# Kernel tuning notes

Measured on AMD Instinct MI355X. Metric: run time of the kernel, lower is better.

The kernel has to match this reference:

```python
import jax, jax.numpy as jnp
import numpy as np
from jax import lax

CUT = 20            # voxel grid per side, hard-coded in the torch module
N, P, OP = 32, 8192, 2048


def _w(key, shape, fan_in):
    return jax.random.normal(key, shape, dtype=jnp.float32) * np.float32(1.0 / np.sqrt(fan_in))


def setup_inputs() -> dict:
    key = jax.random.key(0)
    ks = jax.random.split(key, 20)
    inp = {}
    inp["sc"] = jax.random.uniform(ks[0], (N, P, 2), dtype=jnp.float32, minval=-0.5, maxval=0.5)
    inp["oc"] = jax.random.uniform(ks[1], (N, OP, 2), dtype=jnp.float32, minval=-0.5, maxval=0.5)
    inp["pos"] = jax.random.uniform(ks[2], (N, 2), dtype=jnp.float32, minval=-0.5, maxval=0.5)
    # voxel PointNet MLP (1x1 Conv1d == per-point linear)
    inp["mlp_w1"] = _w(ks[3], (128, 2), 2);        inp["mlp_b1"] = jnp.zeros((128,), jnp.float32)
    inp["mlp_w2"] = _w(ks[4], (256, 128), 128);    inp["mlp_b2"] = jnp.zeros((256,), jnp.float32)
    # dense conv pyramid
    inp["conv1_w"] = _w(ks[5], (512, 256, 3, 3), 256 * 9);   inp["conv1_b"] = jnp.zeros((512,), jnp.float32)
    inp["conv2_w"] = _w(ks[6], (1024, 512, 3, 3), 512 * 9);  inp["conv2_b"] = jnp.zeros((1024,), jnp.float32)
    inp["convt_w"] = _w(ks[7], (512, 1024, 2, 2), 1024 * 4); inp["convt_b"] = jnp.zeros((512,), jnp.float32)
    # object set-abstraction (stack of 1x1 Conv1d)
    inp["sa_w1"] = _w(ks[8], (64, 2), 2);          inp["sa_b1"] = jnp.zeros((64,), jnp.float32)
    inp["sa_w2"] = _w(ks[9], (128, 64), 64);       inp["sa_b2"] = jnp.zeros((128,), jnp.float32)
    inp["sa_w3"] = _w(ks[10], (256, 128), 128);    inp["sa_b3"] = jnp.zeros((256,), jnp.float32)
    inp["sa_w4"] = _w(ks[11], (512, 256), 256);    inp["sa_b4"] = jnp.zeros((512,), jnp.float32)
    # per-cell classifier
    inp["cls_w1"] = _w(ks[12], (1024, 1538), 1538); inp["cls_b1"] = jnp.zeros((1024,), jnp.float32)
    inp["cls_w2"] = _w(ks[13], (256, 1024), 1024);  inp["cls_b2"] = jnp.zeros((256,), jnp.float32)
    inp["cls_w3"] = _w(ks[14], (1, 256), 256);      inp["cls_b3"] = jnp.zeros((1,), jnp.float32)
    return inp


def _conv2d(x, w, b):
    y = lax.conv_general_dilated(x, w, (1, 1), ((1, 1), (1, 1)),
                                 dimension_numbers=("NCHW", "OIHW", "NCHW"))
    return y + b[None, :, None, None]


def _maxpool2(x):
    return lax.reduce_window(x, -jnp.inf, lax.max, (1, 1, 2, 2), (1, 1, 2, 2), "VALID")


def reference(sc, oc, pos,
              mlp_w1, mlp_b1, mlp_w2, mlp_b2,
              conv1_w, conv1_b, conv2_w, conv2_b, convt_w, convt_b,
              sa_w1, sa_b1, sa_w2, sa_b2, sa_w3, sa_b3, sa_w4, sa_b4,
              cls_w1, cls_b1, cls_w2, cls_b2, cls_w3, cls_b3):
    n = sc.shape[0]
    # ---- fused voxelization + PointNet + scatter-max (replaces triple loop) ----
    x, y = sc[..., 0], sc[..., 1]
    # torch condition: cut[i] < x <= cut[i+1] on linspace(-0.5, 0.5, 21)
    bi = jnp.clip(jnp.ceil((x + 0.5) * CUT) - 1, 0, CUT - 1).astype(jnp.int32)
    bj = jnp.clip(jnp.ceil((y + 0.5) * CUT) - 1, 0, CUT - 1).astype(jnp.int32)
    valid = (x > -0.5) & (x <= 0.5) & (y > -0.5) & (y <= 0.5)
    ci = -0.5 + (bi.astype(sc.dtype) + 0.5) / CUT   # voxel center x
    cj = -0.5 + (bj.astype(sc.dtype) + 0.5) / CUT   # voxel center y
    pc = jnp.stack([x - ci, y - cj], axis=-1).reshape(-1, 2)        # [n*P, 2]
    h = jax.nn.relu(pc @ mlp_w1.T + mlp_b1)
    feat = jax.nn.relu(h @ mlp_w2.T + mlp_b2)                       # [n*P, 256]
    seg = jnp.where(valid,
                    jnp.arange(n, dtype=jnp.int32)[:, None] * (CUT * CUT) + bi * CUT + bj,
                    n * CUT * CUT).reshape(-1)                      # invalid -> dummy bin
    nseg = n * CUT * CUT + 1
    mx = jax.ops.segment_max(feat, seg, num_segments=nseg)
    cnt = jax.ops.segment_sum(jnp.ones((n * P,), jnp.float32), seg, num_segments=nseg)
    vox = jnp.where(cnt[:, None] > 0, mx, 0.0)[: n * CUT * CUT]     # empty voxels stay 0
    vox = vox.reshape(n, CUT, CUT, 256).transpose(0, 3, 1, 2)       # [n,256,20,20]
    # ---- dense conv pyramid ----
    f1 = _maxpool2(jax.nn.relu(_conv2d(vox, conv1_w, conv1_b)))     # [n,512,10,10]
    f2 = _maxpool2(jax.nn.relu(_conv2d(f1, conv2_w, conv2_b)))      # [n,1024,5,5]
    f3 = lax.conv_transpose(f2, convt_w, (2, 2), "VALID",
                            dimension_numbers=("NCHW", "OIHW", "NCHW"))
    f3 = f3 + convt_b[None, :, None, None]                          # [n,512,10,10]
    scene = jnp.concatenate([f1, f3], axis=1)                       # [n,1024,10,10]
    S = scene.shape[2]
    scene_flat = scene.reshape(n, 1024, S * S)
    # ---- object PointNet (1x1 convs == per-point linears) + global max ----
    obj_c = oc - jnp.mean(oc, axis=1, keepdims=True)                # [n,OP,2]
    g = jax.nn.relu(obj_c @ sa_w1.T + sa_b1)
    g = jax.nn.relu(g @ sa_w2.T + sa_b2)
    g = jax.nn.relu(g @ sa_w3.T + sa_b3)
    g = jax.nn.relu(g @ sa_w4.T + sa_b4)                            # [n,OP,512]
    obj = jnp.max(g, axis=1)                                        # [n,512]
    obj_tiled = jnp.broadcast_to(obj[:, :, None], (n, 512, S * S))
    # ---- relative position grid ----
    c = -0.5 + (jnp.arange(S, dtype=sc.dtype) + 0.5) / S
    rel_x = jnp.broadcast_to(pos[:, 0][:, None, None] - c[None, :, None], (n, S, S))
    rel_y = jnp.broadcast_to(pos[:, 1][:, None, None] - c[None, None, :], (n, S, S))
    rel = jnp.stack([rel_x, rel_y], axis=1).reshape(n, 2, S * S)
    # ---- per-cell classifier ----
    cin = jnp.concatenate([scene_flat, obj_tiled, rel], axis=1).transpose(0, 2, 1)  # [n,100,1538]
    h = jax.nn.relu(cin @ cls_w1.T + cls_b1)
    h = jax.nn.relu(h @ cls_w2.T + cls_b2)
    return h @ cls_w3.T + cls_b3                                    # [n,100,1]
```

## Files before the change

kernel.cpp:

```cpp
#include <hip/hip_runtime.h>

#define NB 32
#define PP 8192
#define OPP 2048

typedef _Float16 f16;
typedef f16 half8 __attribute__((ext_vector_type(8)));
typedef f16 half4 __attribute__((ext_vector_type(4)));
typedef f16 half2v __attribute__((ext_vector_type(2)));
typedef float f32x4 __attribute__((ext_vector_type(4)));

#define MFMA16(a, b, c) __builtin_amdgcn_mfma_f32_16x16x32_f16(a, b, c, 0, 0, 0)

template <int CO, int CI>
__global__ __launch_bounds__(256) void wfragprep_k(const float* __restrict__ wsrc,
                                                   f16* __restrict__ wf) {
  __shared__ float tile[CI * 9];
  int co = blockIdx.x, t = threadIdx.x;
  const float* src = wsrc + (size_t)co * CI * 9;
  for (int i = t; i < CI * 9; i += 256) tile[i] = src[i];
  __syncthreads();
  constexpr int NBB = CO / 16;
  int nb = co >> 4, l16 = co & 15;
  for (int e = t; e < (CI / 32) * 9 * 4; e += 256) {
    int quad = e & 3;
    int kk = (e >> 2) % 9;
    int cic = e / 36;
    half8 v;
#pragma unroll
    for (int j = 0; j < 8; ++j) {
      int ci = cic * 32 + quad * 8 + j;
      v[j] = (f16)tile[ci * 9 + kk];
    }
    *(half8*)(wf + ((((size_t)cic * 9 + kk) * NBB + nb) * 64 + quad * 16 + l16) * 8) = v;
  }
}

__global__ void cvt16_k(const float* __restrict__ in, f16* __restrict__ out, int n4) {
  int idx = blockIdx.x * 256 + threadIdx.x;
  if (idx >= n4) return;
  float4 v = ((const float4*)in)[idx];
  half4 h; h.x = (f16)v.x; h.y = (f16)v.y; h.z = (f16)v.z; h.w = (f16)v.w;
  ((half4*)out)[idx] = h;
}

__global__ void cw1prep_k(const float* __restrict__ w, f16* __restrict__ out) {
  int idx = blockIdx.x * 256 + threadIdx.x;
  if (idx >= 1024 * 1024) return;
  int co = idx >> 10, k = idx & 1023;
  out[idx] = (f16)w[(size_t)co * 1538 + k];
}

__global__ void ctprep_k(const float* __restrict__ w, f16* __restrict__ out) {
  int idx = blockIdx.x * 256 + threadIdx.x;
  if (idx >= 2048 * 1024) return;
  int j = idx & 7, l = (idx >> 3) & 63, kb = (idx >> 9) & 31, nb = idx >> 14;
  int n16 = l & 15, quad = l >> 4;
  int np = nb * 16 + n16;
  int k = kb * 32 + quad * 8 + j;
  int p = np >> 9, o = np & 511;
  out[idx] = (f16)w[((size_t)o * 1024 + k) * 4 + (3 - p)];
}

__global__ void ocmean_k(const float* __restrict__ oc, float* __restrict__ ocm) {
  int n = blockIdx.x, t = threadIdx.x;
  __shared__ float sx[256], sy[256];
  float ax = 0.f, ay = 0.f;
  for (int p = t; p < OPP; p += 256) {
    ax += oc[((size_t)n * OPP + p) * 2 + 0];
    ay += oc[((size_t)n * OPP + p) * 2 + 1];
  }
  sx[t] = ax; sy[t] = ay;
  __syncthreads();
  for (int s = 128; s > 0; s >>= 1) {
    if (t < s) { sx[t] += sx[t + s]; sy[t] += sy[t + s]; }
    __syncthreads();
  }
  if (t == 0) {
    ocm[n * 2 + 0] = sx[0] / (float)OPP;
    ocm[n * 2 + 1] = sy[0] / (float)OPP;
  }
}

__global__ __launch_bounds__(256) void pointnet_lds_k(
    const float* __restrict__ sc, const float* __restrict__ w1, const float* __restrict__ b1,
    const f16* __restrict__ w2h, const float* __restrict__ b2, float* __restrict__ voxg) {
  __shared__ float voxl[400 * 33];
  int t = threadIdx.x, lane = t & 63, w = t >> 6;
  int quad = lane >> 4, l16 = lane & 15;
  int b = blockIdx.x;
  int ps = b & 3, cg = (b >> 2) & 7, n = b >> 5;
  half2v w1x2[16], w1y2[16], b12[16];
#pragma unroll
  for (int i = 0; i < 16; ++i) {
    int k0 = (i >> 2) * 32 + quad * 8 + (i & 3) * 2;
    w1x2[i] = (half2v){(f16)w1[k0 * 2], (f16)w1[(k0 + 1) * 2]};
    w1y2[i] = (half2v){(f16)w1[k0 * 2 + 1], (f16)w1[(k0 + 1) * 2 + 1]};
    b12[i]  = (half2v){(f16)b1[k0], (f16)b1[k0 + 1]};
  }
  half8 bf[2][4];
  float bias[2];
#pragma unroll
  for (int nt = 0; nt < 2; ++nt) {
    int ch = cg * 32 + nt * 16 + l16;
    bias[nt] = b2[ch];
#pragma unroll
    for (int ks = 0; ks < 4; ++ks)
      bf[nt][ks] = *(const half8*)(w2h + (size_t)ch * 128 + ks * 32 + quad * 8);
  }
  for (int i = t; i < 400 * 33; i += 256) voxl[i] = 0.0f;
  __syncthreads();
  const half2v z2 = {};
  const float* scp = sc + ((size_t)n * PP + (size_t)ps * 2048) * 2;
  int p0 = w * 16 + l16;
  float2 xy = *(const float2*)(scp + p0 * 2);
  for (int it = 0; it < 32; ++it) {
    float x = xy.x, y = xy.y;
    if (it < 31) xy = *(const float2*)(scp + ((it + 1) * 64 + p0) * 2);
    float bif = fminf(fmaxf(ceilf((x + 0.5f) * 20.0f) - 1.0f, 0.0f), 19.0f);
    float bjf = fminf(fmaxf(ceilf((y + 0.5f) * 20.0f) - 1.0f, 0.0f), 19.0f);
    bool valid = (x > -0.5f) && (x <= 0.5f) && (y > -0.5f) && (y <= 0.5f);
    float px = x - (-0.5f + (bif + 0.5f) * 0.05f);
    float py = y - (-0.5f + (bjf + 0.5f) * 0.05f);
    int bn = valid ? ((int)bif * 20 + (int)bjf) : -1;
    f16 pxh = (f16)px, pyh = (f16)py;
    half2v px2 = (half2v){pxh, pxh}, py2 = (half2v){pyh, pyh};
    f32x4 acc0 = {}, acc1 = {};
#pragma unroll
    for (int ks = 0; ks < 4; ++ks) {
      half8 af;
#pragma unroll
      for (int j2 = 0; j2 < 4; ++j2) {
        half2v tmp = w1x2[ks * 4 + j2] * px2 + (w1y2[ks * 4 + j2] * py2 + b12[ks * 4 + j2]);
        tmp = __builtin_elementwise_max(tmp, z2);
        reinterpret_cast<half2v*>(&af)[j2] = tmp;
      }
      acc0 = MFMA16(af, bf[0][ks], acc0);
      acc1 = MFMA16(af, bf[1][ks], acc1);
    }
#pragma unroll
    for (int r = 0; r < 4; ++r) {
      int bn2 = __shfl(bn, quad * 4 + r);
      if (bn2 >= 0) {
        float v0 = fmaxf(acc0[r] + bias[0], 0.0f);
        float v1 = fmaxf(acc1[r] + bias[1], 0.0f);
        atomicMax((int*)voxl + bn2 * 33 + l16, __float_as_int(v0));
        atomicMax((int*)voxl + bn2 * 33 + 16 + l16, __float_as_int(v1));
      }
    }
  }
  __syncthreads();
  float* vg = voxg + ((size_t)n * 400) * 256 + cg * 32;
  for (int i = t; i < 400 * 32; i += 256) {
    int bin = i >> 5, c = i & 31;
    float v = voxl[bin * 33 + c];
    if (v > 0.0f)
      atomicMax((int*)(vg + (size_t)bin * 256) + c, __float_as_int(v));
  }
}

template <int H, int W, int CI, int CO, int MSPLIT>
__global__ __launch_bounds__(256, 2) void convmfma_k(
    const f16* __restrict__ inh, const f16* __restrict__ wf,
    const float* __restrict__ bias, f16* __restrict__ outh) {
  constexpr int HS = H / MSPLIT;
  constexpr int Mpix = HS * W;
  constexpr int MT = (Mpix + 15) / 16;
  constexpr int PR = HS + 2, PC = W + 2;
  constexpr int NCIC = CI / 32;
  constexpr int COG = CO / 128;
  constexpr int NBB = CO / 16;
  extern __shared__ char smem[];
  f16* Ap = (f16*)smem;
  int b = blockIdx.x;
  int cog = b % COG;
  int ms = (b / COG) % MSPLIT;
  int n = b / (COG * MSPLIT);
  int co0 = cog * 128;
  int r0 = ms * HS;
  int t = threadIdx.x, lane = t & 63, w = t >> 6;
  int quad = lane >> 4, l16 = lane & 15;
  int nb0 = cog * 8 + w * 2;

  int abase[MT];
#pragma unroll
  for (int mi = 0; mi < MT; ++mi) {
    int pl = mi * 16 + l16; if (pl > Mpix - 1) pl = Mpix - 1;
    int y = pl / W, x = pl - y * W;
    abase[mi] = (y * PC + x) * 40 + quad * 8;
  }
  f32x4 acc[MT][2] = {};

  const f16* inbase = inh + (size_t)n * H * W * CI;

  for (int cic = 0; cic < NCIC; ++cic) {
    __syncthreads();
    for (int cell = t; cell < PR * PC; cell += 256) {
      int pr = cell / PC, pc = cell - pr * PC;
      int yin = r0 - 1 + pr, xin = pc - 1;
      uint4 d0 = {0,0,0,0}, d1 = {0,0,0,0}, d2 = {0,0,0,0}, d3 = {0,0,0,0};
      if (yin >= 0 && yin < H && xin >= 0 && xin < W) {
        const uint4* src = (const uint4*)(inbase + ((size_t)yin * W + xin) * CI + cic * 32);
        d0 = src[0]; d1 = src[1]; d2 = src[2]; d3 = src[3];
      }
      uint4* dst = (uint4*)(Ap + cell * 40);
      dst[0] = d0; dst[1] = d1; dst[2] = d2; dst[3] = d3;
    }
    __syncthreads();
    const f16* wfc = wf + (size_t)(cic * 9) * NBB * 512;
#pragma unroll
    for (int ky = 0; ky < 3; ++ky)
#pragma unroll
      for (int kx = 0; kx < 3; ++kx) {
        int kk = ky * 3 + kx;
        half8 bf0 = *(const half8*)(wfc + ((size_t)(kk * NBB + nb0) * 64 + lane) * 8);
        half8 bf1 = *(const half8*)(wfc + ((size_t)(kk * NBB + nb0 + 1) * 64 + lane) * 8);
        int shift = (ky * PC + kx) * 40;
#pragma unroll
        for (int mi = 0; mi < MT; ++mi) {
          half8 af = *(const half8*)(Ap + abase[mi] + shift);
          acc[mi][0] = MFMA16(af, bf0, acc[mi][0]);
          acc[mi][1] = MFMA16(af, bf1, acc[mi][1]);
        }
      }
  }
  int co_w = co0 + w * 32;
  float bv0 = bias[co_w + l16];
  float bv1 = bias[co_w + 16 + l16];
  f16* ob = outh + ((size_t)n * H * W + (size_t)ms * Mpix) * CO;
#pragma unroll
  for (int mi = 0; mi < MT; ++mi) {
#pragma unroll
    for (int r = 0; r < 4; ++r) {
      int p = mi * 16 + quad * 4 + r;
      if (p < Mpix) {
        float v0 = acc[mi][0][r] + bv0; v0 = v0 > 0.f ? v0 : 0.f;
        float v1 = acc[mi][1][r] + bv1; v1 = v1 > 0.f ? v1 : 0.f;
        ob[(size_t)p * CO + co_w + l16] = (f16)v0;
        ob[(size_t)p * CO + co_w + 16 + l16] = (f16)v1;
      }
    }
  }
}

__global__ void pool1_k(const f16* __restrict__ g1, f16* __restrict__ f1h,
                        f16* __restrict__ scnh) {
  int idx = blockIdx.x * 256 + threadIdx.x;
  if (idx >= 32 * 100 * 256) return;
  int c2 = idx & 255, rem = idx >> 8;
  int op = rem % 100, n = rem / 100;
  int py = op / 10, px = op - py * 10;
  const f16* base = g1 + (((size_t)n * 400 + (size_t)(2 * py) * 20 + 2 * px) * 512) + c2 * 2;
  float a0 = (float)base[0],   a1 = (float)base[1];
  float b0 = (float)base[512], b1 = (float)base[513];
  const f16* base2 = base + 20 * 512;
  float c0 = (float)base2[0],   c1 = (float)base2[1];
  float d0 = (float)base2[512], d1 = (float)base2[513];
  union { f16 h[2]; unsigned u; } pk;
  pk.h[0] = (f16)fmaxf(fmaxf(a0, b0), fmaxf(c0, d0));
  pk.h[1] = (f16)fmaxf(fmaxf(a1, b1), fmaxf(c1, d1));
  *(unsigned*)(f1h + ((size_t)n * 100 + op) * 512 + c2 * 2) = pk.u;
  *(unsigned*)(scnh + ((size_t)n * 100 + op) * 1024 + c2 * 2) = pk.u;
}

__global__ void pool2_k(const f16* __restrict__ g2, f16* __restrict__ f2h) {
  int idx = blockIdx.x * 256 + threadIdx.x;
  if (idx >= 32 * 25 * 512) return;
  int c2 = idx & 511, rem = idx >> 9;
  int op = rem % 25, n = rem / 25;
  int py = op / 5, px = op - py * 5;
  const f16* base = g2 + (((size_t)n * 100 + (size_t)(2 * py) * 10 + 2 * px) * 1024) + c2 * 2;
  float a0 = (float)base[0],    a1 = (float)base[1];
  float b0 = (float)base[1024], b1 = (float)base[1025];
  const f16* base2 = base + 10 * 1024;
  float c0 = (float)base2[0],    c1 = (float)base2[1];
  float d0 = (float)base2[1024], d1 = (float)base2[1025];
  f16* o = f2h + ((size_t)n * 25 + op) * 1024 + c2 * 2;
  o[0] = (f16)fmaxf(fmaxf(a0, b0), fmaxf(c0, d0));
  o[1] = (f16)fmaxf(fmaxf(a1, b1), fmaxf(c1, d1));
}

__global__ __launch_bounds__(256, 2) void convt_mfma_k(
    const f16* __restrict__ f2h, const f16* __restrict__ ctwf,
    const float* __restrict__ ctb, f16* __restrict__ scnh) {
  __shared__ f16 act[25 * 1048];
  int b = blockIdx.x;
  int ng = b & 15, n = b >> 4;
  int t = threadIdx.x, lane = t & 63, w = t >> 6;
  int quad = lane >> 4, l16 = lane & 15;
  for (int i = t; i < 25 * 128; i += 256) {
    int row = i >> 7, c8 = i & 127;
    *(half8*)(act + row * 1048 + c8 * 8) =
        *(const half8*)(f2h + ((size_t)n * 25 + row) * 1024 + c8 * 8);
  }
  __syncthreads();
  int r1 = 16 + (l16 > 8 ? 8 : l16);
  f32x4 acc[2][2] = {};
  const f16* wp0 = ctwf + ((size_t)((ng * 8 + w * 2 + 0) * 32) * 64 + lane) * 8;
  const f16* wp1 = ctwf + ((size_t)((ng * 8 + w * 2 + 1) * 32) * 64 + lane) * 8;
#pragma unroll 4
  for (int ks = 0; ks < 32; ++ks) {
    half8 a0 = *(const half8*)(act + l16 * 1048 + ks * 32 + quad * 8);
    half8 a1 = *(const half8*)(act + r1 * 1048 + ks * 32 + quad * 8);
    half8 b0 = *(const half8*)(wp0 + (size_t)ks * 512);
    half8 b1 = *(const half8*)(wp1 + (size_t)ks * 512);
    acc[0][0] = MFMA16(a0, b0, acc[0][0]);
    acc[1][0] = MFMA16(a1, b0, acc[1][0]);
    acc[0][1] = MFMA16(a0, b1, acc[0][1]);
    acc[1][1] = MFMA16(a1, b1, acc[1][1]);
  }
#pragma unroll
  for (int nt = 0; nt < 2; ++nt) {
    int np = ng * 128 + w * 32 + nt * 16 + l16;
    int p = np >> 9, co = np & 511;
    int a = p >> 1, bc = p & 1;
    float bb = ctb[co];
#pragma unroll
    for (int mt = 0; mt < 2; ++mt)
#pragma unroll
      for (int r = 0; r < 4; ++r) {
        int px = mt * 16 + quad * 4 + r;
        if (px < 25) {
          int ph = px / 5, pw = px - ph * 5;
          int opx = (2 * ph + a) * 10 + 2 * pw + bc;
          scnh[((size_t)n * 100 + opx) * 1024 + 512 + co] = (f16)(acc[mt][nt][r] + bb);
        }
      }
  }
}

__global__ __launch_bounds__(256, 2) void sa_mfma_k(
    const float* __restrict__ oc, const float* __restrict__ ocm,
    const float* __restrict__ w1, const float* __restrict__ b1,
    const f16* __restrict__ w2h, const float* __restrict__ b2,
    const f16* __restrict__ w3h, const float* __restrict__ b3,
    const f16* __restrict__ w4h, const float* __restrict__ b4,
    float* __restrict__ obj) {
  __shared__ f16 act1[64 * 72];
  __shared__ f16 act2[64 * 136];
  __shared__ f16 act3[64 * 264];
  __shared__ float pcx[64], pcy[64];
  int b = blockIdx.x;
  int n = b >> 5, pb = (b & 31) * 64;
  int t = threadIdx.x, lane = t & 63, w = t >> 6;
  int quad = lane >> 4, l16 = lane & 15;
  if (t < 64) {
    pcx[t] = oc[((size_t)n * OPP + pb + t) * 2 + 0] - ocm[n * 2 + 0];
    pcy[t] = oc[((size_t)n * OPP + pb + t) * 2 + 1] - ocm[n * 2 + 1];
  }
  __syncthreads();
  {
    int c = t & 63, pg = t >> 6;
    float wx = w1[c * 2], wy = w1[c * 2 + 1], bb = b1[c];
#pragma unroll
    for (int j = 0; j < 16; ++j) {
      int p = pg * 16 + j;
      act1[p * 72 + c] = (f16)fmaxf(fmaf(wx, pcx[p], fmaf(wy, pcy[p], bb)), 0.0f);
    }
  }
  __syncthreads();
  {
    int n0 = w * 32;
    f32x4 acc[4][2] = {};
#pragma unroll
    for (int ks = 0; ks < 2; ++ks) {
      half8 a[4];
#pragma unroll
      for (int mt = 0; mt < 4; ++mt)
        a[mt] = *(const half8*)(act1 + (mt * 16 + l16) * 72 + ks * 32 + quad * 8);
#pragma unroll
      for (int nt = 0; nt < 2; ++nt) {
        half8 bf = *(const half8*)(w2h + (size_t)(n0 + nt * 16 + l16) * 64 + ks * 32 + quad * 8);
#pragma unroll
        for (int mt = 0; mt < 4; ++mt)
          acc[mt][nt] = MFMA16(a[mt], bf, acc[mt][nt]);
      }
    }
#pragma unroll
    for (int nt = 0; nt < 2; ++nt) {
      int col = n0 + nt * 16 + l16;
      float bb = b2[col];
#pragma unroll
      for (int mt = 0; mt < 4; ++mt)
#pragma unroll
        for (int r = 0; r < 4; ++r)
          act2[(mt * 16 + quad * 4 + r) * 136 + col] = (f16)fmaxf(acc[mt][nt][r] + bb, 0.0f);
    }
  }
  __syncthreads();
  {
    int n0 = w * 64;
    f32x4 acc[4][4] = {};
#pragma unroll
    for (int ks = 0; ks < 4; ++ks) {
      half8 a[4];
#pragma unroll
      for (int mt = 0; mt < 4; ++mt)
        a[mt] = *(const half8*)(act2 + (mt * 16 + l16) * 136 + ks * 32 + quad * 8);
#pragma unroll
      for (int nt = 0; nt < 4; ++nt) {
        half8 bf = *(const half8*)(w3h + (size_t)(n0 + nt * 16 + l16) * 128 + ks * 32 + quad * 8);
#pragma unroll
        for (int mt = 0; mt < 4; ++mt)
          acc[mt][nt] = MFMA16(a[mt], bf, acc[mt][nt]);
      }
    }
#pragma unroll
    for (int nt = 0; nt < 4; ++nt) {
      int col = n0 + nt * 16 + l16;
      float bb = b3[col];
#pragma unroll
      for (int mt = 0; mt < 4; ++mt)
#pragma unroll
        for (int r = 0; r < 4; ++r)
          act3[(mt * 16 + quad * 4 + r) * 264 + col] = (f16)fmaxf(acc[mt][nt][r] + bb, 0.0f);
    }
  }
  __syncthreads();
  {
    int n0 = w * 128;
    f32x4 acc[4][8] = {};
#pragma unroll
    for (int ks = 0; ks < 8; ++ks) {
      half8 a[4];
#pragma unroll
      for (int mt = 0; mt < 4; ++mt)
        a[mt] = *(const half8*)(act3 + (mt * 16 + l16) * 264 + ks * 32 + quad * 8);
#pragma unroll
      for (int nt = 0; nt < 8; ++nt) {
        half8 bf = *(const half8*)(w4h + (size_t)(n0 + nt * 16 + l16) * 256 + ks * 32 + quad * 8);
#pragma unroll
        for (int mt = 0; mt < 4; ++mt)
          acc[mt][nt] = MFMA16(a[mt], bf, acc[mt][nt]);
      }
    }
#pragma unroll
    for (int nt = 0; nt < 8; ++nt) {
      int col = n0 + nt * 16 + l16;
      float bb = b4[col];
      float v = 0.0f;
#pragma unroll
      for (int mt = 0; mt < 4; ++mt)
#pragma unroll
        for (int r = 0; r < 4; ++r)
          v = fmaxf(v, acc[mt][nt][r] + bb);
      v = fmaxf(v, 0.0f);
      v = fmaxf(v, __shfl_xor(v, 16));
      v = fmaxf(v, __shfl_xor(v, 32));
      if (quad == 0)
        atomicMax((int*)obj + (size_t)n * 512 + col, __float_as_int(v));
    }
  }
}

__global__ __launch_bounds__(256) void cls1_mfma_k(
    const f16* __restrict__ scnh, const float* __restrict__ obj,
    const float* __restrict__ pos, const float* __restrict__ w1raw,
    const f16* __restrict__ w1h, const float* __restrict__ b1,
    f16* __restrict__ h1h) {
  __shared__ f16 act[112 * 72];
  __shared__ float objl[512];
  __shared__ float odl[128], wAl[128], wBl[128];
  int b = blockIdx.x;
  int o8 = b & 7, n = b >> 3;
  int co0 = o8 * 128;
  int t = threadIdx.x, lane = t & 63, w = t >> 6;
  int quad = lane >> 4, l16 = lane & 15;
  objl[t] = obj[(size_t)n * 512 + t];
  objl[t + 256] = obj[(size_t)n * 512 + t + 256];
  __syncthreads();
  if (t < 128) {
    int co = co0 + t;
    const float* wr = w1raw + (size_t)co * 1538;
    float od = 0.0f;
    for (int k = 0; k < 512; ++k) od = fmaf(objl[k], wr[1024 + k], od);
    odl[t] = od + b1[co];
    wAl[t] = wr[1536]; wBl[t] = wr[1537];
  }
  __syncthreads();
  float posx = pos[n * 2 + 0], posy = pos[n * 2 + 1];
  f32x4 acc[7][2];
#pragma unroll
  for (int mt = 0; mt < 7; ++mt)
#pragma unroll
    for (int nt = 0; nt < 2; ++nt) {
      int cl = w * 32 + nt * 16 + l16;
      float od = odl[cl], wA = wAl[cl], wB = wBl[cl];
#pragma unroll
      for (int r = 0; r < 4; ++r) {
        int px = mt * 16 + quad * 4 + r;
        float relx = posx - (-0.5f + ((px / 10) + 0.5f) * 0.1f);
        float rely = posy - (-0.5f + ((px % 10) + 0.5f) * 0.1f);
        acc[mt][nt][r] = od + relx * wA + rely * wB;
      }
    }
  for (int kc = 0; kc < 16; ++kc) {
    int k0 = kc * 64;
    __syncthreads();
    for (int i = t; i < 896; i += 256) {
      int row = i >> 3, c8 = i & 7;
      half8 v = {};
      if (row < 100) v = *(const half8*)(scnh + ((size_t)n * 100 + row) * 1024 + k0 + c8 * 8);
      *(half8*)(act + row * 72 + c8 * 8) = v;
    }
    __syncthreads();
#pragma unroll
    for (int ks = 0; ks < 2; ++ks) {
      half8 bf0 = *(const half8*)(w1h + (size_t)(co0 + w * 32 + l16) * 1024 + k0 + ks * 32 + quad * 8);
      half8 bf1 = *(const half8*)(w1h + (size_t)(co0 + w * 32 + 16 + l16) * 1024 + k0 + ks * 32 + quad * 8);
#pragma unroll
      for (int mt = 0; mt < 7; ++mt) {
        half8 a = *(const half8*)(act + (mt * 16 + l16) * 72 + ks * 32 + quad * 8);
        acc[mt][0] = MFMA16(a, bf0, acc[mt][0]);
        acc[mt][1] = MFMA16(a, bf1, acc[mt][1]);
      }
    }
  }
#pragma unroll
  for (int mt = 0; mt < 7; ++mt)
#pragma unroll
    for (int nt = 0; nt < 2; ++nt) {
      int co = co0 + w * 32 + nt * 16 + l16;
#pragma unroll
      for (int r = 0; r < 4; ++r) {
        int px = mt * 16 + quad * 4 + r;
        if (px < 100)
          h1h[((size_t)n * 100 + px) * 1024 + co] = (f16)fmaxf(acc[mt][nt][r], 0.0f);
      }
    }
}

__global__ __launch_bounds__(256) void cls2_mfma_k(
    const f16* __restrict__ h1h, const f16* __restrict__ w2h16,
    const float* __restrict__ b2, f16* __restrict__ h2h) {
  __shared__ f16 act[64 * 72];
  int b = blockIdx.x;
  int ng = b & 1, mh = (b >> 1) & 1, n = b >> 2;
  int co0 = ng * 128, p0 = mh * 50;
  int t = threadIdx.x, lane = t & 63, w = t >> 6;
  int quad = lane >> 4, l16 = lane & 15;
  f32x4 acc[4][2] = {};
  for (int kc = 0; kc < 16; ++kc) {
    int k0 = kc * 64;
    __syncthreads();
    for (int i = t; i < 512; i += 256) {
      int row = i >> 3, c8 = i & 7;
      int gr = p0 + (row < 50 ? row : 49);
      *(half8*)(act + row * 72 + c8 * 8) =
          *(const half8*)(h1h + ((size_t)n * 100 + gr) * 1024 + k0 + c8 * 8);
    }
    __syncthreads();
#pragma unroll
    for (int ks = 0; ks < 2; ++ks) {
      half8 bf0 = *(const half8*)(w2h16 + (size_t)(co0 + w * 32 + l16) * 1024 + k0 + ks * 32 + quad * 8);
      half8 bf1 = *(const half8*)(w2h16 + (size_t)(co0 + w * 32 + 16 + l16) * 1024 + k0 + ks * 32 + quad * 8);
#pragma unroll
      for (int mt = 0; mt < 4; ++mt) {
        half8 a = *(const half8*)(act + (mt * 16 + l16) * 72 + ks * 32 + quad * 8);
        acc[mt][0] = MFMA16(a, bf0, acc[mt][0]);
        acc[mt][1] = MFMA16(a, bf1, acc[mt][1]);
      }
    }
  }
#pragma unroll
  for (int mt = 0; mt < 4; ++mt)
#pragma unroll
    for (int nt = 0; nt < 2; ++nt) {
      int co = co0 + w * 32 + nt * 16 + l16;
      float bb = b2[co];
#pragma unroll
      for (int r = 0; r < 4; ++r) {
        int pl = mt * 16 + quad * 4 + r;
        if (pl < 50)
          h2h[((size_t)n * 100 + p0 + pl) * 256 + co] = (f16)fmaxf(acc[mt][nt][r] + bb, 0.0f);
      }
    }
}

__global__ void cls3_k(const f16* __restrict__ h2h, const float* __restrict__ w3,
                       const float* __restrict__ b3, float* __restrict__ out) {
  int n = blockIdx.x, t = threadIdx.x;
  if (t < 100) {
    float acc = b3[0];
    const f16* hp = &h2h[((size_t)n * 100 + t) * 256];
    for (int k = 0; k < 256; ++k) acc = fmaf((float)hp[k], w3[k], acc);
    out[n * 100 + t] = acc;
  }
}

extern "C" void kernel_launch(void* const* d_in, const int* in_sizes, int n_in,
                              void* d_out, int out_size, void* d_ws, size_t ws_size,
                              hipStream_t stream) {
  const float* sc      = (const float*)d_in[0];
  const float* oc      = (const float*)d_in[1];
  const float* pos     = (const float*)d_in[2];
  const float* mlp_w1  = (const float*)d_in[3];
  const float* mlp_b1  = (const float*)d_in[4];
  const float* mlp_w2  = (const float*)d_in[5];
  const float* mlp_b2  = (const float*)d_in[6];
  const float* conv1_w = (const float*)d_in[7];
  const float* conv1_b = (const float*)d_in[8];
  const float* conv2_w = (const float*)d_in[9];
  const float* conv2_b = (const float*)d_in[10];
  const float* convt_w = (const float*)d_in[11];
  const float* convt_b = (const float*)d_in[12];
  const float* sa_w1   = (const float*)d_in[13];
  const float* sa_b1   = (const float*)d_in[14];
  const float* sa_w2   = (const float*)d_in[15];
  const float* sa_b2   = (const float*)d_in[16];
  const float* sa_w3   = (const float*)d_in[17];
  const float* sa_b3   = (const float*)d_in[18];
  const float* sa_w4   = (const float*)d_in[19];
  const float* sa_b4   = (const float*)d_in[20];
  const float* cls_w1  = (const float*)d_in[21];
  const float* cls_b1  = (const float*)d_in[22];
  const float* cls_w2  = (const float*)d_in[23];
  const float* cls_b2  = (const float*)d_in[24];
  const float* cls_w3  = (const float*)d_in[25];
  const float* cls_b3  = (const float*)d_in[26];

  float* ws = (float*)d_ws;
  f16*   w1h   = (f16*)ws;
  f16*   w2h   = (f16*)(ws + 589824);
  f16*   mw2h  = (f16*)(ws + 2949120);
  f16*   saw2h = (f16*)(ws + 2965504);
  f16*   saw3h = (f16*)(ws + 2969600);
  f16*   saw4h = (f16*)(ws + 2985984);
  f16*   cw1h  = (f16*)(ws + 3051520);
  f16*   ctwh  = (f16*)(ws + 3575808);
  f16*   cw2h  = (f16*)(ws + 4624384);
  float* big   = ws + 4886528;
  f16*   voxh  = (f16*)(ws + 8163328);
  f16*   f1h   = (f16*)(ws + 8982528);
  f16*   scnh  = (f16*)(ws + 9801728);
  float* obj   = ws + 11440128;
  float* ocm   = ws + 11456512;

  float* voxg  = big;
  f16*   g1buf = (f16*)big;
  f16*   g2buf = (f16*)big;
  f16*   f2h   = voxh;
  f16*   h1h   = w2h;
  f16*   h2h   = scnh;
  float* outp  = (float*)d_out;

  wfragprep_k<512, 256><<<512, 256, 0, stream>>>(conv1_w, w1h);
  wfragprep_k<1024, 512><<<1024, 256, 0, stream>>>(conv2_w, w2h);
  cvt16_k<<<32, 256, 0, stream>>>(mlp_w2, mw2h, 8192);
  cvt16_k<<<8, 256, 0, stream>>>(sa_w2, saw2h, 2048);
  cvt16_k<<<32, 256, 0, stream>>>(sa_w3, saw3h, 8192);
  cvt16_k<<<128, 256, 0, stream>>>(sa_w4, saw4h, 32768);
  cw1prep_k<<<4096, 256, 0, stream>>>(cls_w1, cw1h);
  ctprep_k<<<8192, 256, 0, stream>>>(convt_w, ctwh);
  cvt16_k<<<256, 256, 0, stream>>>(cls_w2, cw2h, 65536);

  hipMemsetAsync(obj, 0, (size_t)16384 * 4, stream);
  hipMemsetAsync(voxg, 0, (size_t)3276800 * 4, stream);
  ocmean_k<<<32, 256, 0, stream>>>(oc, ocm);

  pointnet_lds_k<<<1024, 256, 0, stream>>>(sc, mlp_w1, mlp_b1, mw2h, mlp_b2, voxg);
  cvt16_k<<<3200, 256, 0, stream>>>(voxg, voxh, 819200);

  convmfma_k<20, 20, 256, 512, 4><<<512, 256, 7 * 22 * 80, stream>>>(
      voxh, w1h, conv1_b, g1buf);
  pool1_k<<<3200, 256, 0, stream>>>(g1buf, f1h, scnh);
  convmfma_k<10, 10, 512, 1024, 2><<<512, 256, 7 * 12 * 80, stream>>>(
      f1h, w2h, conv2_b, g2buf);
  pool2_k<<<1600, 256, 0, stream>>>(g2buf, f2h);
  convt_mfma_k<<<512, 256, 0, stream>>>(f2h, ctwh, convt_b, scnh);

  sa_mfma_k<<<1024, 256, 0, stream>>>(oc, ocm, sa_w1, sa_b1, saw2h, sa_b2,
                                      saw3h, sa_b3, saw4h, sa_b4, obj);

  cls1_mfma_k<<<256, 256, 0, stream>>>(scnh, obj, pos, cls_w1, cw1h, cls_b1, h1h);
  cls2_mfma_k<<<128, 256, 0, stream>>>(h1h, cw2h, cls_b2, h2h);
  cls3_k<<<32, 128, 0, stream>>>(h2h, cls_w3, cls_b3, outp);
}
```

Baseline: 499.6 us.

## Split cls1 across pixel quarters and parallelize object-dot over all threads

The cls1 kernel now splits the 100 pixels of each sample into four blocks of 25, so it launches 1024 blocks instead of 256 and needs less LDS and fewer accumulators per block. The per-channel object dot product is split across all 256 threads, two threads per channel, and combined with a shuffle. This gives more parallelism on a GPU with many CUs. In exchange the object dot product is computed four times redundantly, the weight fragments are reloaded per block, and the 32-row tiles waste 7 of 32 rows.

```diff
diff --git a/kernel.cpp b/kernel.cpp
--- a/kernel.cpp
+++ b/kernel.cpp
@@ -458,37 +458,43 @@
     const float* __restrict__ pos, const float* __restrict__ w1raw,
     const f16* __restrict__ w1h, const float* __restrict__ b1,
     f16* __restrict__ h1h) {
-  __shared__ f16 act[112 * 72];
+  __shared__ f16 act[32 * 72];
   __shared__ float objl[512];
   __shared__ float odl[128], wAl[128], wBl[128];
   int b = blockIdx.x;
-  int o8 = b & 7, n = b >> 3;
-  int co0 = o8 * 128;
+  int mq = b & 3, o8 = (b >> 2) & 7, n = b >> 5;
+  int co0 = o8 * 128, p0 = mq * 25;
   int t = threadIdx.x, lane = t & 63, w = t >> 6;
   int quad = lane >> 4, l16 = lane & 15;
   objl[t] = obj[(size_t)n * 512 + t];
   objl[t + 256] = obj[(size_t)n * 512 + t + 256];
   __syncthreads();
-  if (t < 128) {
-    int co = co0 + t;
-    const float* wr = w1raw + (size_t)co * 1538;
+  {
+    int co = co0 + (t >> 1);
+    int kh = (t & 1) * 256;
+    const float* wr = w1raw + (size_t)co * 1538 + 1024 + kh;
     float od = 0.0f;
-    for (int k = 0; k < 512; ++k) od = fmaf(objl[k], wr[1024 + k], od);
-    odl[t] = od + b1[co];
-    wAl[t] = wr[1536]; wBl[t] = wr[1537];
+    for (int k = 0; k < 256; ++k) od = fmaf(objl[kh + k], wr[k], od);
+    od += __shfl_xor(od, 1);
+    if ((t & 1) == 0) {
+      odl[t >> 1] = od + b1[co];
+      wAl[t >> 1] = w1raw[(size_t)co * 1538 + 1536];
+      wBl[t >> 1] = w1raw[(size_t)co * 1538 + 1537];
+    }
   }
   __syncthreads();
   float posx = pos[n * 2 + 0], posy = pos[n * 2 + 1];
-  f32x4 acc[7][2];
-#pragma unroll
-  for (int mt = 0; mt < 7; ++mt)
+  f32x4 acc[2][2];
+#pragma unroll
+  for (int mt = 0; mt < 2; ++mt)
 #pragma unroll
     for (int nt = 0; nt < 2; ++nt) {
       int cl = w * 32 + nt * 16 + l16;
       float od = odl[cl], wA = wAl[cl], wB = wBl[cl];
 #pragma unroll
       for (int r = 0; r < 4; ++r) {
-        int px = mt * 16 + quad * 4 + r;
+        int pl = mt * 16 + quad * 4 + r;
+        int px = p0 + (pl < 25 ? pl : 24);
         float relx = posx - (-0.5f + ((px / 10) + 0.5f) * 0.1f);
         float rely = posy - (-0.5f + ((px % 10) + 0.5f) * 0.1f);
         acc[mt][nt][r] = od + relx * wA + rely * wB;
@@ -497,11 +503,11 @@
   for (int kc = 0; kc < 16; ++kc) {
     int k0 = kc * 64;
     __syncthreads();
-    for (int i = t; i < 896; i += 256) {
-      int row = i >> 3, c8 = i & 7;
-      half8 v = {};
-      if (row < 100) v = *(const half8*)(scnh + ((size_t)n * 100 + row) * 1024 + k0 + c8 * 8);
-      *(half8*)(act + row * 72 + c8 * 8) = v;
+    {
+      int row = t >> 3, c8 = t & 7;
+      int gr = p0 + (row < 25 ? row : 24);
+      *(half8*)(act + row * 72 + c8 * 8) =
+          *(const half8*)(scnh + ((size_t)n * 100 + gr) * 1024 + k0 + c8 * 8);
     }
     __syncthreads();
 #pragma unroll
@@ -509,7 +515,7 @@
       half8 bf0 = *(const half8*)(w1h + (size_t)(co0 + w * 32 + l16) * 1024 + k0 + ks * 32 + quad * 8);
       half8 bf1 = *(const half8*)(w1h + (size_t)(co0 + w * 32 + 16 + l16) * 1024 + k0 + ks * 32 + quad * 8);
 #pragma unroll
-      for (int mt = 0; mt < 7; ++mt) {
+      for (int mt = 0; mt < 2; ++mt) {
         half8 a = *(const half8*)(act + (mt * 16 + l16) * 72 + ks * 32 + quad * 8);
         acc[mt][0] = MFMA16(a, bf0, acc[mt][0]);
         acc[mt][1] = MFMA16(a, bf1, acc[mt][1]);
@@ -517,15 +523,15 @@
     }
   }
 #pragma unroll
-  for (int mt = 0; mt < 7; ++mt)
+  for (int mt = 0; mt < 2; ++mt)
 #pragma unroll
     for (int nt = 0; nt < 2; ++nt) {
       int co = co0 + w * 32 + nt * 16 + l16;
 #pragma unroll
       for (int r = 0; r < 4; ++r) {
-        int px = mt * 16 + quad * 4 + r;
-        if (px < 100)
-          h1h[((size_t)n * 100 + px) * 1024 + co] = (f16)fmaxf(acc[mt][nt][r], 0.0f);
+        int pl = mt * 16 + quad * 4 + r;
+        if (pl < 25)
+          h1h[((size_t)n * 100 + p0 + pl) * 1024 + co] = (f16)fmaxf(acc[mt][nt][r], 0.0f);
       }
     }
 }
@@ -672,7 +678,7 @@
   sa_mfma_k<<<1024, 256, 0, stream>>>(oc, ocm, sa_w1, sa_b1, saw2h, sa_b2,
                                       saw3h, sa_b3, saw4h, sa_b4, obj);
 
-  cls1_mfma_k<<<256, 256, 0, stream>>>(scnh, obj, pos, cls_w1, cw1h, cls_b1, h1h);
+  cls1_mfma_k<<<1024, 256, 0, stream>>>(scnh, obj, pos, cls_w1, cw1h, cls_b1, h1h);
   cls2_mfma_k<<<128, 256, 0, stream>>>(h1h, cw2h, cls_b2, h2h);
   cls3_k<<<32, 128, 0, stream>>>(h2h, cls_w3, cls_b3, outp);
 }
```

Measured after the change: 514.7 us. +3.0%, slower.
